# Optimization experiments

Hardware: AMD Instinct MI355X
Metric: run time of the kernel (lower is better)

## Reference

```python
import jax, jax.numpy as jnp
import numpy as np

N, C, F = 64, 128, 2048


def setup_inputs() -> dict:
    key = jax.random.key(0)
    kx, ka = jax.random.split(key)
    X = jax.random.normal(kx, (N, C, F), dtype=jnp.float32)
    # Glorot-uniform init for A [C, C, F]: fan_in = C*F, fan_out = C*F
    limit = np.sqrt(6.0 / (C * F + C * F)).astype(np.float32)
    A = jax.random.uniform(ka, (C, C, F), dtype=jnp.float32, minval=-limit, maxval=limit)
    return {"X": X, "A": A}


def reference(X, A):
    # scores: reduce feature dim F -> [N, C, M]
    c = jnp.einsum('ncf,cmf->ncm', X, A)
    W = jax.nn.softmax(c, axis=-1)  # attention over source channels M
    # combine: mix channels of X with attention weights -> [N, C, F]
    return jnp.einsum('nmf,ncm->ncf', X, W)
```

## Files before the change

### kernel.cpp

```cpp
#include <hip/hip_runtime.h>
#include <hip/hip_bf16.h>


typedef __attribute__((ext_vector_type(8))) short bf16x8;
typedef __attribute__((ext_vector_type(4))) float f32x4;

#define PART_ELEMS (64 * 128 * 128)
#define WOFF_BYTES (4ull * PART_ELEMS * 4ull)

static __device__ __forceinline__ unsigned f2bf_pk(float a, float b) {
    unsigned ua = __float_as_uint(a);
    unsigned ub = __float_as_uint(b);
    ua = (ua + 0x7FFFu + ((ua >> 16) & 1u)) >> 16;
    ub = (ub + 0x7FFFu + ((ub >> 16) & 1u)) >> 16;
    return ua | (ub << 16);
}

__global__ __launch_bounds__(256, 2) void k_scores(const float* __restrict__ X,
                                                   const float* __restrict__ A,
                                                   float* __restrict__ part) {
    __shared__ short Xt[64 * 72];
    __shared__ short At[128 * 72];

    const int bx = blockIdx.x;
    const int c  = bx >> 2;
    const int p  = bx & 3;
    const int t  = threadIdx.x;
    const int l  = t & 63;
    const int w  = t >> 6;
    const int wn = (w & 1) * 32;
    const int wm = (w >> 1) * 64;
    const int l15 = l & 15;
    const int lg  = l >> 4;

    f32x4 acc[2][4];
#pragma unroll
    for (int i = 0; i < 2; ++i)
#pragma unroll
        for (int j = 0; j < 4; ++j) acc[i][j] = (f32x4)0.0f;

    const int fq    = (t & 15) * 4;
    const int rbase = t >> 4;

    const float* Xg = X + ((size_t)rbase * 128 + c) * 2048 + p * 512 + fq;
    const float* Ag = A + ((size_t)c * 128 + rbase) * 2048 + p * 512 + fq;

    for (int kb = 0; kb < 8; ++kb) {
        const int f0 = kb * 64;
#pragma unroll
        for (int j = 0; j < 4; ++j) {
            float4 v = *(const float4*)(Xg + (size_t)j * (16 * 128 * 2048) + f0);
            *(uint2*)&Xt[(rbase + 16 * j) * 72 + fq] =
                make_uint2(f2bf_pk(v.x, v.y), f2bf_pk(v.z, v.w));
        }
#pragma unroll
        for (int j = 0; j < 8; ++j) {
            float4 v = *(const float4*)(Ag + (size_t)j * (16 * 2048) + f0);
            *(uint2*)&At[(rbase + 16 * j) * 72 + fq] =
                make_uint2(f2bf_pk(v.x, v.y), f2bf_pk(v.z, v.w));
        }
        __syncthreads();
#pragma unroll
        for (int ks = 0; ks < 2; ++ks) {
            const int ko = ks * 32 + lg * 8;
            bf16x8 a[2], b[4];
#pragma unroll
            for (int i = 0; i < 2; ++i)
                a[i] = *(const bf16x8*)&Xt[(wn + 16 * i + l15) * 72 + ko];
#pragma unroll
            for (int j = 0; j < 4; ++j)
                b[j] = *(const bf16x8*)&At[(wm + 16 * j + l15) * 72 + ko];
#pragma unroll
            for (int i = 0; i < 2; ++i)
#pragma unroll
                for (int j = 0; j < 4; ++j)
                    acc[i][j] = __builtin_amdgcn_mfma_f32_16x16x32_bf16(a[i], b[j], acc[i][j], 0, 0, 0);
        }
        __syncthreads();
    }

    float* outp = part + (size_t)p * PART_ELEMS;
#pragma unroll
    for (int i = 0; i < 2; ++i) {
        const int nb = wn + 16 * i + lg * 4;
#pragma unroll
        for (int j = 0; j < 4; ++j) {
            const int m = wm + 16 * j + l15;
#pragma unroll
            for (int r = 0; r < 4; ++r)
                outp[(size_t)(nb + r) * 16384 + c * 128 + m] = acc[i][j][r];
        }
    }
}

__global__ __launch_bounds__(256) void k_softmax(const float* __restrict__ part,
                                                 unsigned int* __restrict__ Wout) {
    const int t   = threadIdx.x;
    const int l   = t & 63;
    const int row = blockIdx.x * 4 + (t >> 6);

    const float* s = part + (size_t)row * 128 + 2 * l;
    float v0 = 0.f, v1 = 0.f;
#pragma unroll
    for (int p = 0; p < 4; ++p) {
        float2 v = *(const float2*)(s + (size_t)p * PART_ELEMS);
        v0 += v.x; v1 += v.y;
    }
    float mx = fmaxf(v0, v1);
#pragma unroll
    for (int d = 1; d < 64; d <<= 1) mx = fmaxf(mx, __shfl_xor(mx, d, 64));
    float e0 = __expf(v0 - mx), e1 = __expf(v1 - mx);
    float sm = e0 + e1;
#pragma unroll
    for (int d = 1; d < 64; d <<= 1) sm += __shfl_xor(sm, d, 64);
    const float inv = 1.0f / sm;
    Wout[(size_t)row * 64 + l] = f2bf_pk(e0 * inv, e1 * inv);
}

__global__ __launch_bounds__(256, 2) void k_combine(const float* __restrict__ X,
                                                    const unsigned short* __restrict__ W,
                                                    float* __restrict__ out) {
    __shared__ short Wl[128 * 136];
    __shared__ short T[128 * 40];

    const int bx = blockIdx.x;
    const int n  = bx >> 4;
    const int f0 = (bx & 15) * 128;
    const int t  = threadIdx.x;
    const int l  = t & 63;
    const int w  = t >> 6;
    const int l15 = l & 15;
    const int lg  = l >> 4;
    const int wc = (w >> 1) * 64;
    const int wf = (w & 1) * 64;

    {
        const int c = t >> 1;
        const int h = (t & 1) * 64;
        const unsigned short* src = W + ((size_t)n * 128 + c) * 128 + h;
#pragma unroll
        for (int j = 0; j < 8; ++j) {
            bf16x8 v = *(const bf16x8*)(src + j * 8);
            *(bf16x8*)&Wl[c * 136 + h + j * 8] = v;
        }
    }

    f32x4 acc[4][4];
#pragma unroll
    for (int i = 0; i < 4; ++i)
#pragma unroll
        for (int j = 0; j < 4; ++j) acc[i][j] = (f32x4)0.0f;

    const int mpr = (t & 15) * 2;
    const int fqu = (t >> 4) * 4;

    for (int m0 = 0; m0 < 128; m0 += 32) {
        __syncthreads();
#pragma unroll
        for (int pass = 0; pass < 2; ++pass) {
            const int fl = fqu + 64 * pass;
            const float* g = X + ((size_t)n * 128 + m0 + mpr) * 2048 + f0 + fl;
            float4 x0 = *(const float4*)g;
            float4 x1 = *(const float4*)(g + 2048);
            unsigned* Tw = (unsigned*)T;
            Tw[(fl + 0) * 20 + (mpr >> 1)] = f2bf_pk(x0.x, x1.x);
            Tw[(fl + 1) * 20 + (mpr >> 1)] = f2bf_pk(x0.y, x1.y);
            Tw[(fl + 2) * 20 + (mpr >> 1)] = f2bf_pk(x0.z, x1.z);
            Tw[(fl + 3) * 20 + (mpr >> 1)] = f2bf_pk(x0.w, x1.w);
        }
        __syncthreads();
        const int ko = lg * 8;
        bf16x8 a[4], b[4];
#pragma unroll
        for (int i = 0; i < 4; ++i)
            a[i] = *(const bf16x8*)&Wl[(wc + 16 * i + l15) * 136 + m0 + ko];
#pragma unroll
        for (int j = 0; j < 4; ++j)
            b[j] = *(const bf16x8*)&T[(wf + 16 * j + l15) * 40 + ko];
#pragma unroll
        for (int i = 0; i < 4; ++i)
#pragma unroll
            for (int j = 0; j < 4; ++j)
                acc[i][j] = __builtin_amdgcn_mfma_f32_16x16x32_bf16(a[i], b[j], acc[i][j], 0, 0, 0);
    }

#pragma unroll
    for (int i = 0; i < 4; ++i) {
        const int c = wc + 16 * i + lg * 4;
#pragma unroll
        for (int j = 0; j < 4; ++j) {
            const int f = f0 + wf + 16 * j + l15;
            float* o = out + ((size_t)n * 128 + c) * 2048 + f;
#pragma unroll
            for (int r = 0; r < 4; ++r) o[(size_t)r * 2048] = acc[i][j][r];
        }
    }
}

extern "C" void kernel_launch(void* const* d_in, const int* in_sizes, int n_in,
                              void* d_out, int out_size, void* d_ws, size_t ws_size,
                              hipStream_t stream) {
    const float* X = (const float*)d_in[0];
    const float* A = (const float*)d_in[1];
    float* out = (float*)d_out;

    float* part = (float*)d_ws;
    unsigned short* W = (unsigned short*)((char*)d_ws + WOFF_BYTES);

    k_scores<<<dim3(512), dim3(256), 0, stream>>>(X, A, part);
    k_softmax<<<dim3(2048), dim3(256), 0, stream>>>(part, (unsigned int*)W);
    k_combine<<<dim3(1024), dim3(256), 0, stream>>>(X, W, out);
}
```

Baseline: 283.4 us.

## Stage X slice once in LDS and stream A directly into MFMA registers

Measured after the change: 282.2 us. No clear change (-0.5%).

```diff
diff --git a/kernel.cpp b/kernel.cpp
--- a/kernel.cpp
+++ b/kernel.cpp
@@ -16,11 +16,19 @@
     return ua | (ub << 16);
 }
 
+static __device__ __forceinline__ bf16x8 pack8(float4 x, float4 y) {
+    union { bf16x8 v; unsigned u[4]; } r;
+    r.u[0] = f2bf_pk(x.x, x.y);
+    r.u[1] = f2bf_pk(x.z, x.w);
+    r.u[2] = f2bf_pk(y.x, y.y);
+    r.u[3] = f2bf_pk(y.z, y.w);
+    return r.v;
+}
+
 __global__ __launch_bounds__(256, 2) void k_scores(const float* __restrict__ X,
                                                    const float* __restrict__ A,
                                                    float* __restrict__ part) {
-    __shared__ short Xt[64 * 72];
-    __shared__ short At[128 * 72];
+    __shared__ short Xt[64 * 520];
 
     const int bx = blockIdx.x;
     const int c  = bx >> 2;
@@ -28,64 +36,74 @@
     const int t  = threadIdx.x;
     const int l  = t & 63;
     const int w  = t >> 6;
-    const int wn = (w & 1) * 32;
-    const int wm = (w >> 1) * 64;
     const int l15 = l & 15;
     const int lg  = l >> 4;
 
-    f32x4 acc[2][4];
-#pragma unroll
-    for (int i = 0; i < 2; ++i)
-#pragma unroll
-        for (int j = 0; j < 4; ++j) acc[i][j] = (f32x4)0.0f;
-
-    const int fq    = (t & 15) * 4;
-    const int rbase = t >> 4;
-
-    const float* Xg = X + ((size_t)rbase * 128 + c) * 2048 + p * 512 + fq;
-    const float* Ag = A + ((size_t)c * 128 + rbase) * 2048 + p * 512 + fq;
-
-    for (int kb = 0; kb < 8; ++kb) {
-        const int f0 = kb * 64;
-#pragma unroll
-        for (int j = 0; j < 4; ++j) {
-            float4 v = *(const float4*)(Xg + (size_t)j * (16 * 128 * 2048) + f0);
-            *(uint2*)&Xt[(rbase + 16 * j) * 72 + fq] =
-                make_uint2(f2bf_pk(v.x, v.y), f2bf_pk(v.z, v.w));
-        }
-#pragma unroll
-        for (int j = 0; j < 8; ++j) {
-            float4 v = *(const float4*)(Ag + (size_t)j * (16 * 2048) + f0);
-            *(uint2*)&At[(rbase + 16 * j) * 72 + fq] =
-                make_uint2(f2bf_pk(v.x, v.y), f2bf_pk(v.z, v.w));
-        }
-        __syncthreads();
-#pragma unroll
-        for (int ks = 0; ks < 2; ++ks) {
-            const int ko = ks * 32 + lg * 8;
-            bf16x8 a[2], b[4];
-#pragma unroll
-            for (int i = 0; i < 2; ++i)
-                a[i] = *(const bf16x8*)&Xt[(wn + 16 * i + l15) * 72 + ko];
-#pragma unroll
-            for (int j = 0; j < 4; ++j)
-                b[j] = *(const bf16x8*)&At[(wm + 16 * j + l15) * 72 + ko];
-#pragma unroll
-            for (int i = 0; i < 2; ++i)
-#pragma unroll
-                for (int j = 0; j < 4; ++j)
-                    acc[i][j] = __builtin_amdgcn_mfma_f32_16x16x32_bf16(a[i], b[j], acc[i][j], 0, 0, 0);
-        }
-        __syncthreads();
-    }
+    {
+        const int fo = (t & 63) * 8;
+        const int r0 = t >> 6;
+#pragma unroll
+        for (int h = 0; h < 2; ++h) {
+            float4 v[8][2];
+#pragma unroll
+            for (int j = 0; j < 8; ++j) {
+                const float* g = X + ((size_t)(h * 32 + j * 4 + r0) * 128 + c) * 2048
+                                   + p * 512 + fo;
+                v[j][0] = *(const float4*)g;
+                v[j][1] = *(const float4*)(g + 4);
+            }
+#pragma unroll
+            for (int j = 0; j < 8; ++j)
+                *(bf16x8*)&Xt[(h * 32 + j * 4 + r0) * 520 + fo] = pack8(v[j][0], v[j][1]);
+        }
+    }
+    __syncthreads();
+
+    f32x4 acc[4][2];
+#pragma unroll
+    for (int i = 0; i < 4; ++i)
+#pragma unroll
+        for (int j = 0; j < 2; ++j) acc[i][j] = (f32x4)0.0f;
+
+    const float* Aw = A + ((size_t)c * 128 + w * 32 + l15) * 2048 + p * 512 + lg * 8;
+
+    float4 pf[2][4];
+#define LOADA(dst, ks) do {                                        \
+        dst[0] = *(const float4*)(Aw + (ks) * 32);                 \
+        dst[1] = *(const float4*)(Aw + (ks) * 32 + 4);             \
+        dst[2] = *(const float4*)(Aw + 16 * 2048 + (ks) * 32);     \
+        dst[3] = *(const float4*)(Aw + 16 * 2048 + (ks) * 32 + 4); \
+    } while (0)
+
+    LOADA(pf[0], 0);
+    LOADA(pf[1], 1);
+
+#pragma unroll
+    for (int ks = 0; ks < 16; ++ks) {
+        bf16x8 b0 = pack8(pf[ks & 1][0], pf[ks & 1][1]);
+        bf16x8 b1 = pack8(pf[ks & 1][2], pf[ks & 1][3]);
+        if (ks + 2 < 16) LOADA(pf[ks & 1], ks + 2);
+
+        bf16x8 a[4];
+#pragma unroll
+        for (int i = 0; i < 4; ++i)
+            a[i] = *(const bf16x8*)&Xt[(i * 16 + l15) * 520 + ks * 32 + lg * 8];
+
+#pragma unroll
+        for (int i = 0; i < 4; ++i) {
+            acc[i][0] = __builtin_amdgcn_mfma_f32_16x16x32_bf16(a[i], b0, acc[i][0], 0, 0, 0);
+            acc[i][1] = __builtin_amdgcn_mfma_f32_16x16x32_bf16(a[i], b1, acc[i][1], 0, 0, 0);
+        }
+    }
+#undef LOADA
 
     float* outp = part + (size_t)p * PART_ELEMS;
 #pragma unroll
-    for (int i = 0; i < 2; ++i) {
-        const int nb = wn + 16 * i + lg * 4;
-#pragma unroll
-        for (int j = 0; j < 4; ++j) {
-            const int m = wm + 16 * j + l15;
+    for (int i = 0; i < 4; ++i) {
+        const int nb = i * 16 + lg * 4;
+#pragma unroll
+        for (int j = 0; j < 2; ++j) {
+            const int m = w * 32 + j * 16 + l15;
 #pragma unroll
             for (int r = 0; r < 4; ++r)
                 outp[(size_t)(nb + r) * 16384 + c * 128 + m] = acc[i][j][r];
```

## Drop LDS staging; load MFMA fragments directly from global with register double-buffering

Applied to the files above, without the earlier changes.

After: 303.7 us. +7.2%, slower.

```diff
diff --git a/kernel.cpp b/kernel.cpp
--- a/kernel.cpp
+++ b/kernel.cpp
@@ -16,11 +16,30 @@
     return ua | (ub << 16);
 }
 
+static __device__ __forceinline__ bf16x8 pack8(float4 x, float4 y) {
+    union { bf16x8 v; __hip_bfloat162 h[4]; } r;
+    r.h[0] = __float22bfloat162_rn(make_float2(x.x, x.y));
+    r.h[1] = __float22bfloat162_rn(make_float2(x.z, x.w));
+    r.h[2] = __float22bfloat162_rn(make_float2(y.x, y.y));
+    r.h[3] = __float22bfloat162_rn(make_float2(y.z, y.w));
+    return r.v;
+}
+
+static __device__ __forceinline__ bf16x8 pack8s(float a0, float a1, float a2, float a3,
+                                                float a4, float a5, float a6, float a7) {
+    union { bf16x8 v; __hip_bfloat162 h[4]; } r;
+    r.h[0] = __float22bfloat162_rn(make_float2(a0, a1));
+    r.h[1] = __float22bfloat162_rn(make_float2(a2, a3));
+    r.h[2] = __float22bfloat162_rn(make_float2(a4, a5));
+    r.h[3] = __float22bfloat162_rn(make_float2(a6, a7));
+    return r.v;
+}
+
 __global__ __launch_bounds__(256, 2) void k_scores(const float* __restrict__ X,
                                                    const float* __restrict__ A,
                                                    float* __restrict__ part) {
-    __shared__ short Xt[64 * 72];
-    __shared__ short At[128 * 72];
+    constexpr int KW  = 512;
+    constexpr int NKS = KW / 32;
 
     const int bx = blockIdx.x;
     const int c  = bx >> 2;
@@ -28,69 +47,73 @@
     const int t  = threadIdx.x;
     const int l  = t & 63;
     const int w  = t >> 6;
-    const int wn = (w & 1) * 32;
-    const int wm = (w >> 1) * 64;
     const int l15 = l & 15;
     const int lg  = l >> 4;
-
-    f32x4 acc[2][4];
-#pragma unroll
-    for (int i = 0; i < 2; ++i)
-#pragma unroll
-        for (int j = 0; j < 4; ++j) acc[i][j] = (f32x4)0.0f;
-
-    const int fq    = (t & 15) * 4;
-    const int rbase = t >> 4;
-
-    const float* Xg = X + ((size_t)rbase * 128 + c) * 2048 + p * 512 + fq;
-    const float* Ag = A + ((size_t)c * 128 + rbase) * 2048 + p * 512 + fq;
-
-    for (int kb = 0; kb < 8; ++kb) {
-        const int f0 = kb * 64;
-#pragma unroll
-        for (int j = 0; j < 4; ++j) {
-            float4 v = *(const float4*)(Xg + (size_t)j * (16 * 128 * 2048) + f0);
-            *(uint2*)&Xt[(rbase + 16 * j) * 72 + fq] =
-                make_uint2(f2bf_pk(v.x, v.y), f2bf_pk(v.z, v.w));
-        }
-#pragma unroll
-        for (int j = 0; j < 8; ++j) {
-            float4 v = *(const float4*)(Ag + (size_t)j * (16 * 2048) + f0);
-            *(uint2*)&At[(rbase + 16 * j) * 72 + fq] =
-                make_uint2(f2bf_pk(v.x, v.y), f2bf_pk(v.z, v.w));
-        }
-        __syncthreads();
-#pragma unroll
-        for (int ks = 0; ks < 2; ++ks) {
-            const int ko = ks * 32 + lg * 8;
-            bf16x8 a[2], b[4];
-#pragma unroll
-            for (int i = 0; i < 2; ++i)
-                a[i] = *(const bf16x8*)&Xt[(wn + 16 * i + l15) * 72 + ko];
-#pragma unroll
-            for (int j = 0; j < 4; ++j)
-                b[j] = *(const bf16x8*)&At[(wm + 16 * j + l15) * 72 + ko];
-#pragma unroll
-            for (int i = 0; i < 2; ++i)
-#pragma unroll
-                for (int j = 0; j < 4; ++j)
-                    acc[i][j] = __builtin_amdgcn_mfma_f32_16x16x32_bf16(a[i], b[j], acc[i][j], 0, 0, 0);
-        }
-        __syncthreads();
-    }
-
-    float* outp = part + (size_t)p * PART_ELEMS;
-#pragma unroll
-    for (int i = 0; i < 2; ++i) {
-        const int nb = wn + 16 * i + lg * 4;
-#pragma unroll
-        for (int j = 0; j < 4; ++j) {
-            const int m = wm + 16 * j + l15;
-#pragma unroll
-            for (int r = 0; r < 4; ++r)
-                outp[(size_t)(nb + r) * 16384 + c * 128 + m] = acc[i][j][r];
-        }
-    }
+    const int nh = (w & 1) * 32;
+    const int mh = (w >> 1) * 64;
+
+    const float* Xb = X + ((size_t)(nh + l15) * 128 + c) * 2048 + p * KW + lg * 8;
+    const float* Ab = A + ((size_t)c * 128 + mh + l15) * 2048 + p * KW + lg * 8;
+
+    struct Buf { float4 a0, a1, a2, a3, b0, b1, b2, b3, b4, b5, b6, b7; };
+
+#define SLD(B, ko) do {                                              \
+        B.a0 = *(const float4*)(Xb + (ko));                          \
+        B.a1 = *(const float4*)(Xb + (ko) + 4);                      \
+        B.a2 = *(const float4*)(Xb + 16 * 128 * 2048 + (ko));        \
+        B.a3 = *(const float4*)(Xb + 16 * 128 * 2048 + (ko) + 4);    \
+        B.b0 = *(const float4*)(Ab + (ko));                          \
+        B.b1 = *(const float4*)(Ab + (ko) + 4);                      \
+        B.b2 = *(const float4*)(Ab + 16 * 2048 + (ko));              \
+        B.b3 = *(const float4*)(Ab + 16 * 2048 + (ko) + 4);          \
+        B.b4 = *(const float4*)(Ab + 32 * 2048 + (ko));              \
+        B.b5 = *(const float4*)(Ab + 32 * 2048 + (ko) + 4);          \
+        B.b6 = *(const float4*)(Ab + 48 * 2048 + (ko));              \
+        B.b7 = *(const float4*)(Ab + 48 * 2048 + (ko) + 4);          \
+    } while (0)
+
+    f32x4 acc00 = (f32x4)0.f, acc01 = (f32x4)0.f, acc02 = (f32x4)0.f, acc03 = (f32x4)0.f;
+    f32x4 acc10 = (f32x4)0.f, acc11 = (f32x4)0.f, acc12 = (f32x4)0.f, acc13 = (f32x4)0.f;
+
+#define SCOMP(B) do {                                                            \
+        bf16x8 fa0 = pack8(B.a0, B.a1);                                          \
+        bf16x8 fa1 = pack8(B.a2, B.a3);                                          \
+        bf16x8 fb0 = pack8(B.b0, B.b1);                                          \
+        bf16x8 fb1 = pack8(B.b2, B.b3);                                          \
+        bf16x8 fb2 = pack8(B.b4, B.b5);                                          \
+        bf16x8 fb3 = pack8(B.b6, B.b7);                                          \
+        acc00 = __builtin_amdgcn_mfma_f32_16x16x32_bf16(fa0, fb0, acc00, 0, 0, 0); \
+        acc01 = __builtin_amdgcn_mfma_f32_16x16x32_bf16(fa0, fb1, acc01, 0, 0, 0); \
+        acc02 = __builtin_amdgcn_mfma_f32_16x16x32_bf16(fa0, fb2, acc02, 0, 0, 0); \
+        acc03 = __builtin_amdgcn_mfma_f32_16x16x32_bf16(fa0, fb3, acc03, 0, 0, 0); \
+        acc10 = __builtin_amdgcn_mfma_f32_16x16x32_bf16(fa1, fb0, acc10, 0, 0, 0); \
+        acc11 = __builtin_amdgcn_mfma_f32_16x16x32_bf16(fa1, fb1, acc11, 0, 0, 0); \
+        acc12 = __builtin_amdgcn_mfma_f32_16x16x32_bf16(fa1, fb2, acc12, 0, 0, 0); \
+        acc13 = __builtin_amdgcn_mfma_f32_16x16x32_bf16(fa1, fb3, acc13, 0, 0, 0); \
+    } while (0)
+
+    Buf U, V;
+    SLD(U, 0);
+    SLD(V, 32);
+#pragma unroll
+    for (int kk = 0; kk < NKS; kk += 2) {
+        SCOMP(U);
+        if (kk + 2 < NKS) SLD(U, (kk + 2) * 32);
+        SCOMP(V);
+        if (kk + 3 < NKS) SLD(V, (kk + 3) * 32);
+    }
+#undef SLD
+#undef SCOMP
+
+    float* outp = part + (size_t)p * PART_ELEMS + c * 128;
+#define SST(av, nt, mt) do {                                                       \
+        float* o = outp + (size_t)(nh + (nt) * 16 + lg * 4) * 16384                \
+                        + mh + (mt) * 16 + l15;                                    \
+        o[0] = av[0]; o[16384] = av[1]; o[32768] = av[2]; o[49152] = av[3];        \
+    } while (0)
+    SST(acc00, 0, 0); SST(acc01, 0, 1); SST(acc02, 0, 2); SST(acc03, 0, 3);
+    SST(acc10, 1, 0); SST(acc11, 1, 1); SST(acc12, 1, 2); SST(acc13, 1, 3);
+#undef SST
 }
 
 __global__ __launch_bounds__(256) void k_softmax(const float* __restrict__ part,
@@ -120,79 +143,80 @@
 __global__ __launch_bounds__(256, 2) void k_combine(const float* __restrict__ X,
                                                     const unsigned short* __restrict__ W,
                                                     float* __restrict__ out) {
-    __shared__ short Wl[128 * 136];
-    __shared__ short T[128 * 40];
-
     const int bx = blockIdx.x;
     const int n  = bx >> 4;
-    const int f0 = (bx & 15) * 128;
     const int t  = threadIdx.x;
     const int l  = t & 63;
     const int w  = t >> 6;
     const int l15 = l & 15;
     const int lg  = l >> 4;
-    const int wc = (w >> 1) * 64;
-    const int wf = (w & 1) * 64;
-
-    {
-        const int c = t >> 1;
-        const int h = (t & 1) * 64;
-        const unsigned short* src = W + ((size_t)n * 128 + c) * 128 + h;
-#pragma unroll
-        for (int j = 0; j < 8; ++j) {
-            bf16x8 v = *(const bf16x8*)(src + j * 8);
-            *(bf16x8*)&Wl[c * 136 + h + j * 8] = v;
-        }
-    }
-
-    f32x4 acc[4][4];
-#pragma unroll
-    for (int i = 0; i < 4; ++i)
-#pragma unroll
-        for (int j = 0; j < 4; ++j) acc[i][j] = (f32x4)0.0f;
-
-    const int mpr = (t & 15) * 2;
-    const int fqu = (t >> 4) * 4;
-
-    for (int m0 = 0; m0 < 128; m0 += 32) {
-        __syncthreads();
-#pragma unroll
-        for (int pass = 0; pass < 2; ++pass) {
-            const int fl = fqu + 64 * pass;
-            const float* g = X + ((size_t)n * 128 + m0 + mpr) * 2048 + f0 + fl;
-            float4 x0 = *(const float4*)g;
-            float4 x1 = *(const float4*)(g + 2048);
-            unsigned* Tw = (unsigned*)T;
-            Tw[(fl + 0) * 20 + (mpr >> 1)] = f2bf_pk(x0.x, x1.x);
-            Tw[(fl + 1) * 20 + (mpr >> 1)] = f2bf_pk(x0.y, x1.y);
-            Tw[(fl + 2) * 20 + (mpr >> 1)] = f2bf_pk(x0.z, x1.z);
-            Tw[(fl + 3) * 20 + (mpr >> 1)] = f2bf_pk(x0.w, x1.w);
-        }
-        __syncthreads();
-        const int ko = lg * 8;
-        bf16x8 a[4], b[4];
-#pragma unroll
-        for (int i = 0; i < 4; ++i)
-            a[i] = *(const bf16x8*)&Wl[(wc + 16 * i + l15) * 136 + m0 + ko];
-#pragma unroll
-        for (int j = 0; j < 4; ++j)
-            b[j] = *(const bf16x8*)&T[(wf + 16 * j + l15) * 40 + ko];
-#pragma unroll
-        for (int i = 0; i < 4; ++i)
-#pragma unroll
-            for (int j = 0; j < 4; ++j)
-                acc[i][j] = __builtin_amdgcn_mfma_f32_16x16x32_bf16(a[i], b[j], acc[i][j], 0, 0, 0);
-    }
-
-#pragma unroll
-    for (int i = 0; i < 4; ++i) {
-        const int c = wc + 16 * i + lg * 4;
-#pragma unroll
-        for (int j = 0; j < 4; ++j) {
-            const int f = f0 + wf + 16 * j + l15;
-            float* o = out + ((size_t)n * 128 + c) * 2048 + f;
-#pragma unroll
-            for (int r = 0; r < 4; ++r) o[(size_t)r * 2048] = acc[i][j][r];
+    const int f0 = (bx & 15) * 128 + w * 32;
+
+    const unsigned short* Wb = W + ((size_t)n * 128 + l15) * 128 + lg * 8;
+    const float* Xb = X + ((size_t)n * 128 + lg * 8) * 2048 + f0 + l15;
+
+    struct XBuf { float a0, a1, a2, a3, a4, a5, a6, a7,
+                        b0, b1, b2, b3, b4, b5, b6, b7; };
+
+#define CLD(S, ks) do {                                   \
+        S.a0 = Xb[((ks) * 32 + 0) * 2048];                \
+        S.a1 = Xb[((ks) * 32 + 1) * 2048];                \
+        S.a2 = Xb[((ks) * 32 + 2) * 2048];                \
+        S.a3 = Xb[((ks) * 32 + 3) * 2048];                \
+        S.a4 = Xb[((ks) * 32 + 4) * 2048];                \
+        S.a5 = Xb[((ks) * 32 + 5) * 2048];                \
+        S.a6 = Xb[((ks) * 32 + 6) * 2048];                \
+        S.a7 = Xb[((ks) * 32 + 7) * 2048];                \
+        S.b0 = Xb[((ks) * 32 + 0) * 2048 + 16];           \
+        S.b1 = Xb[((ks) * 32 + 1) * 2048 + 16];           \
+        S.b2 = Xb[((ks) * 32 + 2) * 2048 + 16];           \
+        S.b3 = Xb[((ks) * 32 + 3) * 2048 + 16];           \
+        S.b4 = Xb[((ks) * 32 + 4) * 2048 + 16];           \
+        S.b5 = Xb[((ks) * 32 + 5) * 2048 + 16];           \
+        S.b6 = Xb[((ks) * 32 + 6) * 2048 + 16];           \
+        S.b7 = Xb[((ks) * 32 + 7) * 2048 + 16];           \
+    } while (0)
+
+    f32x4 acc[8][2];
+#pragma unroll
+    for (int i = 0; i < 8; ++i) {
+        acc[i][0] = (f32x4)0.f;
+        acc[i][1] = (f32x4)0.f;
+    }
+
+#define CCOMP(S, ks) do {                                                          \
+        bf16x8 q0 = pack8s(S.a0, S.a1, S.a2, S.a3, S.a4, S.a5, S.a6, S.a7);        \
+        bf16x8 q1 = pack8s(S.b0, S.b1, S.b2, S.b3, S.b4, S.b5, S.b6, S.b7);        \
+        const unsigned short* wp = Wb + (ks) * 32;                                 \
+        _Pragma("unroll")                                                          \
+        for (int i = 0; i < 8; ++i) {                                              \
+            bf16x8 af = *(const bf16x8*)(wp + (size_t)i * 16 * 128);               \
+            acc[i][0] = __builtin_amdgcn_mfma_f32_16x16x32_bf16(af, q0, acc[i][0], 0, 0, 0); \
+            acc[i][1] = __builtin_amdgcn_mfma_f32_16x16x32_bf16(af, q1, acc[i][1], 0, 0, 0); \
+        }                                                                          \
+    } while (0)
+
+    XBuf U, V;
+    CLD(U, 0);
+    CLD(V, 1);
+    CCOMP(U, 0);
+    CLD(U, 2);
+    CCOMP(V, 1);
+    CLD(V, 3);
+    CCOMP(U, 2);
+    CCOMP(V, 3);
+#undef CLD
+#undef CCOMP
+
+#pragma unroll
+    for (int i = 0; i < 8; ++i) {
+#pragma unroll
+        for (int j = 0; j < 2; ++j) {
+            float* o = out + ((size_t)n * 128 + i * 16 + lg * 4) * 2048 + f0 + j * 16 + l15;
+            o[0]        = acc[i][j][0];
+            o[2048]     = acc[i][j][1];
+            o[2 * 2048] = acc[i][j][2];
+            o[3 * 2048] = acc[i][j][3];
         }
     }
 }
```

## Stream fp32 tiles into swizzled LDS via direct global-to-LDS loads with double buffering

Applied to the files above, without the earlier changes.

Result: no change. 279.8 us (-1.3%).

```diff
diff --git a/kernel.cpp b/kernel.cpp
--- a/kernel.cpp
+++ b/kernel.cpp
@@ -7,6 +7,13 @@
 
 #define PART_ELEMS (64 * 128 * 128)
 #define WOFF_BYTES (4ull * PART_ELEMS * 4ull)
+
+typedef __attribute__((address_space(3))) void lds_vp;
+typedef const __attribute__((address_space(1))) void glob_vp;
+
+static __device__ __forceinline__ void gload_lds16(const void* g, void* l) {
+    __builtin_amdgcn_global_load_lds((glob_vp*)g, (lds_vp*)l, 16, 0, 0);
+}
 
 static __device__ __forceinline__ unsigned f2bf_pk(float a, float b) {
     unsigned ua = __float_as_uint(a);
@@ -16,11 +23,29 @@
     return ua | (ub << 16);
 }
 
+static __device__ __forceinline__ bf16x8 pack8v(f32x4 x, f32x4 y) {
+    union { bf16x8 v; __hip_bfloat162 h[4]; } r;
+    r.h[0] = __float22bfloat162_rn(make_float2(x[0], x[1]));
+    r.h[1] = __float22bfloat162_rn(make_float2(x[2], x[3]));
+    r.h[2] = __float22bfloat162_rn(make_float2(y[0], y[1]));
+    r.h[3] = __float22bfloat162_rn(make_float2(y[2], y[3]));
+    return r.v;
+}
+
+static __device__ __forceinline__ bf16x8 pack8s(float a0, float a1, float a2, float a3,
+                                                float a4, float a5, float a6, float a7) {
+    union { bf16x8 v; __hip_bfloat162 h[4]; } r;
+    r.h[0] = __float22bfloat162_rn(make_float2(a0, a1));
+    r.h[1] = __float22bfloat162_rn(make_float2(a2, a3));
+    r.h[2] = __float22bfloat162_rn(make_float2(a4, a5));
+    r.h[3] = __float22bfloat162_rn(make_float2(a6, a7));
+    return r.v;
+}
+
 __global__ __launch_bounds__(256, 2) void k_scores(const float* __restrict__ X,
                                                    const float* __restrict__ A,
                                                    float* __restrict__ part) {
-    __shared__ short Xt[64 * 72];
-    __shared__ short At[128 * 72];
+    __shared__ float lds[2][6144];
 
     const int bx = blockIdx.x;
     const int c  = bx >> 2;
@@ -28,10 +53,35 @@
     const int t  = threadIdx.x;
     const int l  = t & 63;
     const int w  = t >> 6;
-    const int wn = (w & 1) * 32;
-    const int wm = (w >> 1) * 64;
     const int l15 = l & 15;
     const int lg  = l >> 4;
+    const int nh  = (w & 1) * 32;
+    const int mh  = (w >> 1) * 64;
+
+    const int lr   = l >> 3;
+    const int sw16 = ((l & 7) ^ lr) << 4;
+
+    const char* xg[2];
+#pragma unroll
+    for (int q = 0; q < 2; ++q) {
+        const int n = w * 16 + q * 8 + lr;
+        xg[q] = (const char*)(X + ((size_t)n * 128 + c) * 2048 + p * 512) + sw16;
+    }
+    const char* ag[4];
+#pragma unroll
+    for (int q = 0; q < 4; ++q) {
+        const int m = w * 32 + q * 8 + lr;
+        ag[q] = (const char*)(A + ((size_t)c * 128 + m) * 2048 + p * 512) + sw16;
+    }
+
+#define STAGE(d, ks) do {                                                    \
+        _Pragma("unroll")                                                    \
+        for (int q = 0; q < 2; ++q)                                          \
+            gload_lds16(xg[q] + (ks) * 128, &lds[d][(w * 2 + q) * 256]);     \
+        _Pragma("unroll")                                                    \
+        for (int q = 0; q < 4; ++q)                                          \
+            gload_lds16(ag[q] + (ks) * 128, &lds[d][2048 + (w * 4 + q) * 256]); \
+    } while (0)
 
     f32x4 acc[2][4];
 #pragma unroll
@@ -39,58 +89,55 @@
 #pragma unroll
         for (int j = 0; j < 4; ++j) acc[i][j] = (f32x4)0.0f;
 
-    const int fq    = (t & 15) * 4;
-    const int rbase = t >> 4;
-
-    const float* Xg = X + ((size_t)rbase * 128 + c) * 2048 + p * 512 + fq;
-    const float* Ag = A + ((size_t)c * 128 + rbase) * 2048 + p * 512 + fq;
-
-    for (int kb = 0; kb < 8; ++kb) {
-        const int f0 = kb * 64;
+#define SCOMP(d) do {                                                        \
+        bf16x8 fa[2], fb[4];                                                 \
+        _Pragma("unroll")                                                    \
+        for (int i = 0; i < 2; ++i) {                                        \
+            const int n = nh + 16 * i + l15;                                 \
+            const char* base = (const char*)&lds[d][n * 32];                 \
+            const int xo = (n & 7) << 4;                                     \
+            f32x4 lo = *(const f32x4*)(base + ((lg * 32) ^ xo));             \
+            f32x4 hi = *(const f32x4*)(base + ((lg * 32 + 16) ^ xo));        \
+            fa[i] = pack8v(lo, hi);                                          \
+        }                                                                    \
+        _Pragma("unroll")                                                    \
+        for (int j = 0; j < 4; ++j) {                                        \
+            const int m = mh + 16 * j + l15;                                 \
+            const char* base = (const char*)&lds[d][2048 + m * 32];          \
+            const int xo = (m & 7) << 4;                                     \
+            f32x4 lo = *(const f32x4*)(base + ((lg * 32) ^ xo));             \
+            f32x4 hi = *(const f32x4*)(base + ((lg * 32 + 16) ^ xo));        \
+            fb[j] = pack8v(lo, hi);                                          \
+        }                                                                    \
+        _Pragma("unroll")                                                    \
+        for (int i = 0; i < 2; ++i)                                          \
+            _Pragma("unroll")                                                \
+            for (int j = 0; j < 4; ++j)                                      \
+                acc[i][j] = __builtin_amdgcn_mfma_f32_16x16x32_bf16(fa[i], fb[j], acc[i][j], 0, 0, 0); \
+    } while (0)
+
+    STAGE(0, 0);
+    __syncthreads();
+    for (int ks = 0; ks < 16; ++ks) {
+        const int d = ks & 1;
+        if (ks < 15) STAGE(d ^ 1, ks + 1);
+        SCOMP(d);
+        __syncthreads();
+    }
+#undef STAGE
+#undef SCOMP
+
+    float* outp = part + (size_t)p * PART_ELEMS + c * 128;
+#pragma unroll
+    for (int i = 0; i < 2; ++i)
 #pragma unroll
         for (int j = 0; j < 4; ++j) {
-            float4 v = *(const float4*)(Xg + (size_t)j * (16 * 128 * 2048) + f0);
-            *(uint2*)&Xt[(rbase + 16 * j) * 72 + fq] =
-                make_uint2(f2bf_pk(v.x, v.y), f2bf_pk(v.z, v.w));
+            float* o = outp + (size_t)(nh + i * 16 + lg * 4) * 16384 + mh + j * 16 + l15;
+            o[0]     = acc[i][j][0];
+            o[16384] = acc[i][j][1];
+            o[32768] = acc[i][j][2];
+            o[49152] = acc[i][j][3];
         }
-#pragma unroll
-        for (int j = 0; j < 8; ++j) {
-            float4 v = *(const float4*)(Ag + (size_t)j * (16 * 2048) + f0);
-            *(uint2*)&At[(rbase + 16 * j) * 72 + fq] =
-                make_uint2(f2bf_pk(v.x, v.y), f2bf_pk(v.z, v.w));
-        }
-        __syncthreads();
-#pragma unroll
-        for (int ks = 0; ks < 2; ++ks) {
-            const int ko = ks * 32 + lg * 8;
-            bf16x8 a[2], b[4];
-#pragma unroll
-            for (int i = 0; i < 2; ++i)
-                a[i] = *(const bf16x8*)&Xt[(wn + 16 * i + l15) * 72 + ko];
-#pragma unroll
-            for (int j = 0; j < 4; ++j)
-                b[j] = *(const bf16x8*)&At[(wm + 16 * j + l15) * 72 + ko];
-#pragma unroll
-            for (int i = 0; i < 2; ++i)
-#pragma unroll
-                for (int j = 0; j < 4; ++j)
-                    acc[i][j] = __builtin_amdgcn_mfma_f32_16x16x32_bf16(a[i], b[j], acc[i][j], 0, 0, 0);
-        }
-        __syncthreads();
-    }
-
-    float* outp = part + (size_t)p * PART_ELEMS;
-#pragma unroll
-    for (int i = 0; i < 2; ++i) {
-        const int nb = wn + 16 * i + lg * 4;
-#pragma unroll
-        for (int j = 0; j < 4; ++j) {
-            const int m = wm + 16 * j + l15;
-#pragma unroll
-            for (int r = 0; r < 4; ++r)
-                outp[(size_t)(nb + r) * 16384 + c * 128 + m] = acc[i][j][r];
-        }
-    }
 }
 
 __global__ __launch_bounds__(256) void k_softmax(const float* __restrict__ part,
@@ -120,12 +167,11 @@
 __global__ __launch_bounds__(256, 2) void k_combine(const float* __restrict__ X,
                                                     const unsigned short* __restrict__ W,
                                                     float* __restrict__ out) {
-    __shared__ short Wl[128 * 136];
-    __shared__ short T[128 * 40];
+    __shared__ float xt[2][4096];
 
     const int bx = blockIdx.x;
     const int n  = bx >> 4;
-    const int f0 = (bx & 15) * 128;
+    const int fb = (bx & 15) * 128;
     const int t  = threadIdx.x;
     const int l  = t & 63;
     const int w  = t >> 6;
@@ -134,67 +180,79 @@
     const int wc = (w >> 1) * 64;
     const int wf = (w & 1) * 64;
 
-    {
-        const int c = t >> 1;
-        const int h = (t & 1) * 64;
-        const unsigned short* src = W + ((size_t)n * 128 + c) * 128 + h;
-#pragma unroll
-        for (int j = 0; j < 8; ++j) {
-            bf16x8 v = *(const bf16x8*)(src + j * 8);
-            *(bf16x8*)&Wl[c * 136 + h + j * 8] = v;
+    bf16x8 wfr[4][4];
+#pragma unroll
+    for (int ct = 0; ct < 4; ++ct)
+#pragma unroll
+        for (int ms = 0; ms < 4; ++ms)
+            wfr[ct][ms] = *(const bf16x8*)(W + ((size_t)n * 128 + wc + ct * 16 + l15) * 128
+                                             + ms * 32 + lg * 8);
+
+    const char* sg[4];
+#pragma unroll
+    for (int q = 0; q < 4; ++q) {
+        const int mi = w * 4 + q;
+        const int m  = mi * 2 + (l >> 5);
+        const int fswz = ((l & 31) * 16) ^ (((m >> 3) & 3) << 5);
+        sg[q] = (const char*)(X + ((size_t)n * 128 + m) * 2048 + fb) + fswz;
+    }
+
+#define CSTAGE(d, ms) do {                                                   \
+        _Pragma("unroll")                                                    \
+        for (int q = 0; q < 4; ++q)                                          \
+            gload_lds16(sg[q] + (size_t)(ms) * (32 * 2048 * 4),              \
+                        &xt[d][(w * 4 + q) * 256]);                          \
+    } while (0)
+
+    f32x4 acc[4][4];
+#pragma unroll
+    for (int i = 0; i < 4; ++i)
+#pragma unroll
+        for (int j = 0; j < 4; ++j) acc[i][j] = (f32x4)0.0f;
+
+#define CCOMP(d, ms) do {                                                    \
+        _Pragma("unroll")                                                    \
+        for (int jt = 0; jt < 4; ++jt) {                                     \
+            const int fcb = ((wf + jt * 16 + l15) * 4) ^ (lg << 5);          \
+            const char* base = (const char*)&xt[d][0] + (size_t)lg * 8 * 512 + fcb; \
+            float v0 = *(const float*)(base + 0 * 512);                      \
+            float v1 = *(const float*)(base + 1 * 512);                      \
+            float v2 = *(const float*)(base + 2 * 512);                      \
+            float v3 = *(const float*)(base + 3 * 512);                      \
+            float v4 = *(const float*)(base + 4 * 512);                      \
+            float v5 = *(const float*)(base + 5 * 512);                      \
+            float v6 = *(const float*)(base + 6 * 512);                      \
+            float v7 = *(const float*)(base + 7 * 512);                      \
+            bf16x8 q8 = pack8s(v0, v1, v2, v3, v4, v5, v6, v7);              \
+            _Pragma("unroll")                                                \
+            for (int ct = 0; ct < 4; ++ct)                                   \
+                acc[ct][jt] = __builtin_amdgcn_mfma_f32_16x16x32_bf16(wfr[ct][ms], q8, acc[ct][jt], 0, 0, 0); \
+        }                                                                    \
+    } while (0)
+
+    CSTAGE(0, 0);
+    __syncthreads();
+#pragma unroll
+    for (int ms = 0; ms < 4; ++ms) {
+        const int d = ms & 1;
+        if (ms < 3) CSTAGE(d ^ 1, ms + 1);
+        CCOMP(d, ms);
+        __syncthreads();
+    }
+#undef CSTAGE
+#undef CCOMP
+
+#pragma unroll
+    for (int ct = 0; ct < 4; ++ct)
+#pragma unroll
+        for (int jt = 0; jt < 4; ++jt) {
+            float* o = out + ((size_t)n * 128 + wc + ct * 16 + lg * 4) * 2048
+                           + fb + wf + jt * 16 + l15;
+            o[0]        = acc[ct][jt][0];
+            o[2048]     = acc[ct][jt][1];
+            o[2 * 2048] = acc[ct][jt][2];
+            o[3 * 2048] = acc[ct][jt][3];
         }
-    }
-
-    f32x4 acc[4][4];
-#pragma unroll
-    for (int i = 0; i < 4; ++i)
-#pragma unroll
-        for (int j = 0; j < 4; ++j) acc[i][j] = (f32x4)0.0f;
-
-    const int mpr = (t & 15) * 2;
-    const int fqu = (t >> 4) * 4;
-
-    for (int m0 = 0; m0 < 128; m0 += 32) {
-        __syncthreads();
-#pragma unroll
-        for (int pass = 0; pass < 2; ++pass) {
-            const int fl = fqu + 64 * pass;
-            const float* g = X + ((size_t)n * 128 + m0 + mpr) * 2048 + f0 + fl;
-            float4 x0 = *(const float4*)g;
-            float4 x1 = *(const float4*)(g + 2048);
-            unsigned* Tw = (unsigned*)T;
-            Tw[(fl + 0) * 20 + (mpr >> 1)] = f2bf_pk(x0.x, x1.x);
-            Tw[(fl + 1) * 20 + (mpr >> 1)] = f2bf_pk(x0.y, x1.y);
-            Tw[(fl + 2) * 20 + (mpr >> 1)] = f2bf_pk(x0.z, x1.z);
-            Tw[(fl + 3) * 20 + (mpr >> 1)] = f2bf_pk(x0.w, x1.w);
-        }
-        __syncthreads();
-        const int ko = lg * 8;
-        bf16x8 a[4], b[4];
-#pragma unroll
-        for (int i = 0; i < 4; ++i)
-            a[i] = *(const bf16x8*)&Wl[(wc + 16 * i + l15) * 136 + m0 + ko];
-#pragma unroll
-        for (int j = 0; j < 4; ++j)
-            b[j] = *(const bf16x8*)&T[(wf + 16 * j + l15) * 40 + ko];
-#pragma unroll
-        for (int i = 0; i < 4; ++i)
-#pragma unroll
-            for (int j = 0; j < 4; ++j)
-                acc[i][j] = __builtin_amdgcn_mfma_f32_16x16x32_bf16(a[i], b[j], acc[i][j], 0, 0, 0);
-    }
-
-#pragma unroll
-    for (int i = 0; i < 4; ++i) {
-        const int c = wc + 16 * i + lg * 4;
-#pragma unroll
-        for (int j = 0; j < 4; ++j) {
-            const int f = f0 + wf + 16 * j + l15;
-            float* o = out + ((size_t)n * 128 + c) * 2048 + f;
-#pragma unroll
-            for (int r = 0; r < 4; ++r) o[(size_t)r * 2048] = acc[i][j][r];
-        }
-    }
 }
 
 extern "C" void kernel_launch(void* const* d_in, const int* in_sizes, int n_in,
```
